# Optimization experiments

Hardware: AMD Instinct MI355X
Metric: run time of the kernel (lower is better)

## Reference

```python
import jax, jax.numpy as jnp
import numpy as np

HIDDEN = 1024
HEADS = 16
HEAD_DIM = HIDDEN // HEADS
B, L = 4, 2048


def setup_inputs() -> dict:
    key = jax.random.key(0)
    ks = jax.random.split(key, 9)
    s = 1.0 / np.sqrt(HIDDEN)
    inp = {
        "x": jax.random.normal(ks[0], (B, L, HIDDEN), dtype=jnp.float32),
        "wq": jax.random.uniform(ks[1], (HIDDEN, HIDDEN), jnp.float32, -s, s),
        "bq": jax.random.uniform(ks[2], (HIDDEN,), jnp.float32, -s, s),
        "wk": jax.random.uniform(ks[3], (HIDDEN, HIDDEN), jnp.float32, -s, s),
        "bk": jax.random.uniform(ks[4], (HIDDEN,), jnp.float32, -s, s),
        "wv": jax.random.uniform(ks[5], (HIDDEN, HIDDEN), jnp.float32, -s, s),
        "bv": jax.random.uniform(ks[6], (HIDDEN,), jnp.float32, -s, s),
        "wo": jax.random.uniform(ks[7], (HIDDEN, HIDDEN), jnp.float32, -s, s),
        "bo": jax.random.uniform(ks[8], (HIDDEN,), jnp.float32, -s, s),
    }
    return inp


def reference(x, wq, bq, wk, bk, wv, bv, wo, bo):
    b, l, d = x.shape
    # projections (torch Linear: x @ W^T + b; here weights stored as [in,out])
    q = x @ wq + bq
    k = x @ wk + bk
    v = x @ wv + bv
    # [b, h, l, hd]
    q = q.reshape(b, l, HEADS, HEAD_DIM).transpose(0, 2, 1, 3)
    k = k.reshape(b, l, HEADS, HEAD_DIM).transpose(0, 2, 1, 3)
    v = v.reshape(b, l, HEADS, HEAD_DIM).transpose(0, 2, 1, 3)
    scale = 1.0 / np.sqrt(HEAD_DIM).astype(np.float32)
    score = jnp.einsum('bhqd,bhkd->bhqk', q, k) * scale
    attn = jax.nn.softmax(score, axis=-1)
    out = jnp.einsum('bhqk,bhkd->bhqd', attn, v)
    out = out.transpose(0, 2, 1, 3).reshape(b, l, d)
    return out @ wo + bo
```

## Files before the change

kernel.cpp:

```cpp
#include <hip/hip_runtime.h>
#include <hip/hip_bf16.h>
#include <cstdint>

#define HIDDEN 1024
#define HEADS 16
#define HEAD_DIM 64
#define BATCH 4
#define SEQ 2048
#define TOK (BATCH * SEQ)

typedef __attribute__((ext_vector_type(8))) short short8;
typedef __attribute__((ext_vector_type(4))) float f32x4;
typedef __attribute__((ext_vector_type(16))) float f32x16;

__device__ __forceinline__ void gload_lds16(const void* g, void* s) {
  __builtin_amdgcn_global_load_lds(
      (const __attribute__((address_space(1))) void*)g,
      (__attribute__((address_space(3))) void*)s, 16, 0, 0);
}

__device__ __forceinline__ unsigned short f2bf(float x) {
  union { __hip_bfloat16 h; unsigned short u; } c;
  c.h = __float2bfloat16(x);
  return c.u;
}

__global__ __launch_bounds__(256) void convert_f32_bf16(
    const float* __restrict__ in, __hip_bfloat16* __restrict__ out, int n4) {
  int idx = blockIdx.x * blockDim.x + threadIdx.x;
  int stride = gridDim.x * blockDim.x;
  for (int i = idx; i < n4; i += stride) {
    float4 v = ((const float4*)in)[i];
    union { ushort4 u; __hip_bfloat16 h[4]; } r;
    r.h[0] = __float2bfloat16(v.x);
    r.h[1] = __float2bfloat16(v.y);
    r.h[2] = __float2bfloat16(v.z);
    r.h[3] = __float2bfloat16(v.w);
    ((ushort4*)out)[i] = r.u;
  }
}

__global__ __launch_bounds__(256) void transpose_to_bf16(
    const float* __restrict__ in, __hip_bfloat16* __restrict__ out) {
  __shared__ __hip_bfloat16 t[64][65];
  const int tx = threadIdx.x & 63;
  const int ty = threadIdx.x >> 6;
  const int k0 = blockIdx.y * 64;
  const int n0 = blockIdx.x * 64;
#pragma unroll
  for (int i = 0; i < 16; ++i) {
    int r = i * 4 + ty;
    t[r][tx] = __float2bfloat16(in[(size_t)(k0 + r) * 1024 + n0 + tx]);
  }
  __syncthreads();
#pragma unroll
  for (int i = 0; i < 16; ++i) {
    int r = i * 4 + ty;
    out[(size_t)(n0 + r) * 1024 + k0 + tx] = t[tx][r];
  }
}

template <int EPI, int KDIM>
__global__ __launch_bounds__(256) void gemm128(
    const __hip_bfloat16* __restrict__ A, const __hip_bfloat16* __restrict__ Bt,
    float* __restrict__ Cout, const float* __restrict__ bias,
    const float* __restrict__ bq, const float* __restrict__ bk,
    const float* __restrict__ bv, __hip_bfloat16* __restrict__ Qb,
    __hip_bfloat16* __restrict__ Kb, __hip_bfloat16* __restrict__ VTb) {
  __shared__ __hip_bfloat16 As[128 * 32];
  __shared__ __hip_bfloat16 Bs[128 * 32];
  const int tid = threadIdx.x;
  const int w = tid >> 6, l = tid & 63;
  const int lc = l & 15, lg = l >> 4;
  const int wr = w >> 1, wc = w & 1;
  const int bm0 = blockIdx.x * 128;
  const int bn0 = blockIdx.y * 128;
  const int lrow = l >> 2;
  const int lk = (l & 3) * 8;

  f32x4 acc[4][4] = {};

#pragma unroll 1
  for (int kt = 0; kt < KDIM; kt += 32) {
    if (w < 2) {
#pragma unroll
      for (int i = 0; i < 4; ++i) {
        int rloc = w * 64 + i * 16;
        const __hip_bfloat16* src =
            A + (size_t)(bm0 + rloc + lrow) * KDIM + kt + lk;
        gload_lds16(src, &As[rloc * 32]);
      }
    } else {
#pragma unroll
      for (int i = 0; i < 4; ++i) {
        int rloc = (w - 2) * 64 + i * 16;
        const __hip_bfloat16* src =
            Bt + (size_t)(bn0 + rloc + lrow) * KDIM + kt + lk;
        gload_lds16(src, &Bs[rloc * 32]);
      }
    }
    __syncthreads();
    short8 af[4], bf[4];
#pragma unroll
    for (int mt = 0; mt < 4; ++mt)
      af[mt] = *(const short8*)&As[(wr * 64 + mt * 16 + lc) * 32 + 8 * lg];
#pragma unroll
    for (int nt = 0; nt < 4; ++nt)
      bf[nt] = *(const short8*)&Bs[(wc * 64 + nt * 16 + lc) * 32 + 8 * lg];
#pragma unroll
    for (int mt = 0; mt < 4; ++mt)
#pragma unroll
      for (int nt = 0; nt < 4; ++nt)
        acc[mt][nt] = __builtin_amdgcn_mfma_f32_16x16x32_bf16(
            af[mt], bf[nt], acc[mt][nt], 0, 0, 0);
    __syncthreads();
  }

#pragma unroll
  for (int mt = 0; mt < 4; ++mt) {
#pragma unroll
    for (int nt = 0; nt < 4; ++nt) {
#pragma unroll
      for (int r = 0; r < 4; ++r) {
        int m = bm0 + wr * 64 + mt * 16 + 4 * lg + r;
        int n = bn0 + wc * 64 + nt * 16 + lc;
        float v = acc[mt][nt][r];
        if (EPI == 0) {
          Cout[(size_t)m * 1024 + n] = v + bias[n];
        } else {
          int proj = n >> 10, win = n & 1023, h = win >> 6, d = win & 63;
          const float* bp = (proj == 0) ? bq : ((proj == 1) ? bk : bv);
          __hip_bfloat16 hv = __float2bfloat16(v + bp[win]);
          int b = m >> 11, lq = m & 2047;
          if (proj == 0)
            Qb[((size_t)(b * 16 + h) * 2048 + lq) * 64 + d] = hv;
          else if (proj == 1)
            Kb[((size_t)(b * 16 + h) * 2048 + lq) * 64 + d] = hv;
          else
            VTb[((size_t)(b * 16 + h) * 64 + d) * 2048 + lq] = hv;
        }
      }
    }
  }
}

__global__ __launch_bounds__(256, 2) void attn32(
    const __hip_bfloat16* __restrict__ Qb, const __hip_bfloat16* __restrict__ Kb,
    const __hip_bfloat16* __restrict__ VTb, __hip_bfloat16* __restrict__ AO) {
  __shared__ __align__(16) char lds[2][2][8192];
  const int tid = threadIdx.x;
  const int w = tid >> 6, l = tid & 63;
  const int q32 = l & 31;
  const int hi = l >> 5;
  const int bh = blockIdx.y;
  const int qb = blockIdx.x;
  const int b = bh >> 4, h = bh & 15;

  const __hip_bfloat16* Qp = Qb + (size_t)bh * SEQ * 64;
  const char* Kg = (const char*)(Kb + (size_t)bh * SEQ * 64);
  const char* Vg = (const char*)(VTb + (size_t)bh * 64 * SEQ);

  const int q0w = qb * 128 + w * 32;
  short8 qf[4];
#pragma unroll
  for (int ds = 0; ds < 4; ++ds)
    qf[ds] = *(const short8*)(Qp + (size_t)(q0w + q32) * 64 + ds * 16 + 8 * hi);

  const int srow = l >> 3;
  const int scol = (16 * (l & 7)) ^ (srow << 4);
  const int i0 = 2 * w, i1 = 2 * w + 1;

#define STAGE_KV(buf, kv0)                                                   \
  {                                                                          \
    gload_lds16(Kg + (size_t)((kv0) + i0 * 8 + srow) * 128 + scol,           \
                &lds[buf][0][i0 * 1024]);                                    \
    gload_lds16(Kg + (size_t)((kv0) + i1 * 8 + srow) * 128 + scol,           \
                &lds[buf][0][i1 * 1024]);                                    \
    gload_lds16(Vg + (size_t)(i0 * 8 + srow) * (SEQ * 2) +                   \
                    (size_t)(kv0) * 2 + scol,                                \
                &lds[buf][1][i0 * 1024]);                                    \
    gload_lds16(Vg + (size_t)(i1 * 8 + srow) * (SEQ * 2) +                   \
                    (size_t)(kv0) * 2 + scol,                                \
                &lds[buf][1][i1 * 1024]);                                    \
  }

  STAGE_KV(0, 0);

  f32x16 o0 = {}, o1 = {};
  float mrun = -INFINITY, lrun = 0.0f;
  const float cs = 0.125f * 1.44269504088896f;
  const int swz = (q32 & 7) << 4;

#pragma unroll 1
  for (int it = 0; it < 32; ++it) {
    const int kv0 = it * 64;
    const int cur = it & 1;
    __syncthreads();
    if (it < 31) STAGE_KV(cur ^ 1, kv0 + 64);

    const char* Kt = lds[cur][0];
    f32x16 s0 = {}, s1 = {};
#pragma unroll
    for (int ds = 0; ds < 4; ++ds) {
      const int c = (32 * ds + 16 * hi) ^ swz;
      short8 k0 = *(const short8*)(Kt + q32 * 128 + c);
      short8 k1 = *(const short8*)(Kt + (32 + q32) * 128 + c);
      s0 = __builtin_amdgcn_mfma_f32_32x32x16_bf16(k0, qf[ds], s0, 0, 0, 0);
      s1 = __builtin_amdgcn_mfma_f32_32x32x16_bf16(k1, qf[ds], s1, 0, 0, 0);
    }

    float tm[8];
#pragma unroll
    for (int i = 0; i < 8; ++i)
      tm[i] = fmaxf(fmaxf(s0[2 * i], s0[2 * i + 1]),
                    fmaxf(s1[2 * i], s1[2 * i + 1]));
    float t = fmaxf(fmaxf(fmaxf(tm[0], tm[1]), fmaxf(tm[2], tm[3])),
                    fmaxf(fmaxf(tm[4], tm[5]), fmaxf(tm[6], tm[7])));
    t = fmaxf(t, __shfl_xor(t, 32));

    const float mn = fmaxf(mrun, t * cs);
    const float corr = exp2f(mrun - mn);
    mrun = mn;

    float p0[16], p1[16];
    float rs = 0.0f;
#pragma unroll
    for (int i = 0; i < 16; ++i) {
      p0[i] = exp2f(fmaf(s0[i], cs, -mn));
      p1[i] = exp2f(fmaf(s1[i], cs, -mn));
      rs += p0[i] + p1[i];
    }
    rs += __shfl_xor(rs, 32);
    lrun = lrun * corr + rs;

    uint32_t pw[4][4];
#pragma unroll
    for (int ks = 0; ks < 4; ++ks) {
      const int base = 8 * (ks & 1);
#pragma unroll
      for (int g = 0; g < 4; ++g) {
        float lo = (ks < 2) ? p0[base + 2 * g] : p1[base + 2 * g];
        float hp = (ks < 2) ? p0[base + 2 * g + 1] : p1[base + 2 * g + 1];
        pw[ks][g] = (uint32_t)f2bf(lo) | ((uint32_t)f2bf(hp) << 16);
      }
    }

    o0 *= corr;
    o1 *= corr;

    const char* Vt = lds[cur][1];
#pragma unroll
    for (int ks = 0; ks < 4; ++ks) {
      union { short8 v; uint32_t u[4]; } pb;
      pb.u[0] = pw[ks][0];
      pb.u[1] = pw[ks][1];
      pb.u[2] = pw[ks][2];
      pb.u[3] = pw[ks][3];
      const int cA = (32 * ks + 8 * hi) ^ swz;
      const int cB = (32 * ks + 16 + 8 * hi) ^ swz;
      union { short8 v; uint64_t u[2]; } a0, a1;
      a0.u[0] = *(const uint64_t*)(Vt + q32 * 128 + cA);
      a0.u[1] = *(const uint64_t*)(Vt + q32 * 128 + cB);
      a1.u[0] = *(const uint64_t*)(Vt + (32 + q32) * 128 + cA);
      a1.u[1] = *(const uint64_t*)(Vt + (32 + q32) * 128 + cB);
      o0 = __builtin_amdgcn_mfma_f32_32x32x16_bf16(a0.v, pb.v, o0, 0, 0, 0);
      o1 = __builtin_amdgcn_mfma_f32_32x32x16_bf16(a1.v, pb.v, o1, 0, 0, 0);
    }
  }

  const float rinv = 1.0f / lrun;
  const size_t orow = (size_t)(b * SEQ + q0w + q32) * 1024 + h * 64;
#pragma unroll
  for (int g = 0; g < 4; ++g) {
    ushort4 c0, c1;
    c0.x = f2bf(o0[4 * g + 0] * rinv);
    c0.y = f2bf(o0[4 * g + 1] * rinv);
    c0.z = f2bf(o0[4 * g + 2] * rinv);
    c0.w = f2bf(o0[4 * g + 3] * rinv);
    c1.x = f2bf(o1[4 * g + 0] * rinv);
    c1.y = f2bf(o1[4 * g + 1] * rinv);
    c1.z = f2bf(o1[4 * g + 2] * rinv);
    c1.w = f2bf(o1[4 * g + 3] * rinv);
    *(ushort4*)(AO + orow + 8 * g + 4 * hi) = c0;
    *(ushort4*)(AO + orow + 32 + 8 * g + 4 * hi) = c1;
  }
#undef STAGE_KV
}

extern "C" void kernel_launch(void* const* d_in, const int* in_sizes, int n_in,
                              void* d_out, int out_size, void* d_ws,
                              size_t ws_size, hipStream_t stream) {
  const float* x = (const float*)d_in[0];
  const float* wq = (const float*)d_in[1];
  const float* bq = (const float*)d_in[2];
  const float* wk = (const float*)d_in[3];
  const float* bk = (const float*)d_in[4];
  const float* wv = (const float*)d_in[5];
  const float* bv = (const float*)d_in[6];
  const float* wo = (const float*)d_in[7];
  const float* bo = (const float*)d_in[8];
  float* out = (float*)d_out;
  char* ws = (char*)d_ws;

  __hip_bfloat16* XB = (__hip_bfloat16*)(ws);
  __hip_bfloat16* WT = (__hip_bfloat16*)(ws + (16ull << 20));
  __hip_bfloat16* WOT = (__hip_bfloat16*)(ws + (22ull << 20));
  __hip_bfloat16* QB = (__hip_bfloat16*)(ws + (24ull << 20));
  __hip_bfloat16* KB = (__hip_bfloat16*)(ws + (40ull << 20));
  __hip_bfloat16* VTB = (__hip_bfloat16*)(ws + (56ull << 20));
  __hip_bfloat16* AO = XB;

  convert_f32_bf16<<<2048, 256, 0, stream>>>(x, XB, TOK * HIDDEN / 4);
  transpose_to_bf16<<<dim3(16, 16), 256, 0, stream>>>(wq, WT);
  transpose_to_bf16<<<dim3(16, 16), 256, 0, stream>>>(wk, WT + 1024 * 1024);
  transpose_to_bf16<<<dim3(16, 16), 256, 0, stream>>>(wv, WT + 2 * 1024 * 1024);
  transpose_to_bf16<<<dim3(16, 16), 256, 0, stream>>>(wo, WOT);

  gemm128<1, 1024><<<dim3(64, 24), 256, 0, stream>>>(
      XB, WT, nullptr, nullptr, bq, bk, bv, QB, KB, VTB);

  attn32<<<dim3(16, 64), 256, 0, stream>>>(QB, KB, VTB, AO);

  gemm128<0, 1024><<<dim3(64, 8), 256, 0, stream>>>(
      AO, WOT, out, bo, nullptr, nullptr, nullptr, nullptr, nullptr, nullptr);
}
```

Before: 368.6 us.

## Lazy softmax rescale, packed bf16 converts, max3 reductions, higher attention occupancy

The attention kernel skips the running-max update and the output/denominator rescale when every lane's new tile max stays within 8 (log2 units) of the running max, using a wave vote. Probability and output bf16 packing switches to the hardware v_cvt_pk_bf16_f32 instruction, and the max reduction is restructured into three-input max chains. Launch bounds are raised from 2 to 4 blocks per CU. Together these aim to cut VALU work in the softmax path, at the cost of possible register pressure or spills from the tighter occupancy bound and larger exponent values (up to 2^8) before normalisation.

Result: faster. 349.4 us (-5.2%).

```diff
diff --git a/kernel.cpp b/kernel.cpp
--- a/kernel.cpp
+++ b/kernel.cpp
@@ -23,6 +23,12 @@
   union { __hip_bfloat16 h; unsigned short u; } c;
   c.h = __float2bfloat16(x);
   return c.u;
+}
+
+__device__ __forceinline__ uint32_t cvt_pk_bf16(float lo, float hi) {
+  uint32_t r;
+  asm("v_cvt_pk_bf16_f32 %0, %1, %2" : "=v"(r) : "v"(lo), "v"(hi));
+  return r;
 }
 
 __global__ __launch_bounds__(256) void convert_f32_bf16(
@@ -144,7 +150,7 @@
   }
 }
 
-__global__ __launch_bounds__(256, 2) void attn32(
+__global__ __launch_bounds__(256, 4) void attn32(
     const __hip_bfloat16* __restrict__ Qb, const __hip_bfloat16* __restrict__ Kb,
     const __hip_bfloat16* __restrict__ VTb, __hip_bfloat16* __restrict__ AO) {
   __shared__ __align__(16) char lds[2][2][8192];
@@ -209,18 +215,26 @@
       s1 = __builtin_amdgcn_mfma_f32_32x32x16_bf16(k1, qf[ds], s1, 0, 0, 0);
     }
 
-    float tm[8];
-#pragma unroll
-    for (int i = 0; i < 8; ++i)
-      tm[i] = fmaxf(fmaxf(s0[2 * i], s0[2 * i + 1]),
-                    fmaxf(s1[2 * i], s1[2 * i + 1]));
-    float t = fmaxf(fmaxf(fmaxf(tm[0], tm[1]), fmaxf(tm[2], tm[3])),
-                    fmaxf(fmaxf(tm[4], tm[5]), fmaxf(tm[6], tm[7])));
+#define M3F(a, b, c) fmaxf(fmaxf((a), (b)), (c))
+    float u0 = M3F(s0[0], s0[1], s0[2]);
+    float u1 = M3F(s0[3], s0[4], s0[5]);
+    float u2 = M3F(s0[6], s0[7], s0[8]);
+    float u3 = M3F(s0[9], s0[10], s0[11]);
+    float u4 = M3F(s0[12], s0[13], s0[14]);
+    float u5 = M3F(s0[15], s1[0], s1[1]);
+    float u6 = M3F(s1[2], s1[3], s1[4]);
+    float u7 = M3F(s1[5], s1[6], s1[7]);
+    float u8 = M3F(s1[8], s1[9], s1[10]);
+    float u9 = M3F(s1[11], s1[12], s1[13]);
+    float ua = fmaxf(s1[14], s1[15]);
+    float t =
+        M3F(M3F(u0, u1, u2), M3F(u3, u4, u5), M3F(M3F(u6, u7, u8), u9, ua));
+#undef M3F
     t = fmaxf(t, __shfl_xor(t, 32));
-
-    const float mn = fmaxf(mrun, t * cs);
-    const float corr = exp2f(mrun - mn);
-    mrun = mn;
+    const float tl = t * cs;
+
+    const bool nores = (__all(tl <= mrun + 8.0f) != 0);
+    const float mn = nores ? mrun : fmaxf(mrun, tl);
 
     float p0[16], p1[16];
     float rs = 0.0f;
@@ -231,7 +245,15 @@
       rs += p0[i] + p1[i];
     }
     rs += __shfl_xor(rs, 32);
-    lrun = lrun * corr + rs;
+
+    if (!nores) {
+      const float corr = exp2f(mrun - mn);
+      mrun = mn;
+      lrun *= corr;
+      o0 *= corr;
+      o1 *= corr;
+    }
+    lrun += rs;
 
     uint32_t pw[4][4];
 #pragma unroll
@@ -241,12 +263,9 @@
       for (int g = 0; g < 4; ++g) {
         float lo = (ks < 2) ? p0[base + 2 * g] : p1[base + 2 * g];
         float hp = (ks < 2) ? p0[base + 2 * g + 1] : p1[base + 2 * g + 1];
-        pw[ks][g] = (uint32_t)f2bf(lo) | ((uint32_t)f2bf(hp) << 16);
+        pw[ks][g] = cvt_pk_bf16(lo, hp);
       }
     }
-
-    o0 *= corr;
-    o1 *= corr;
 
     const char* Vt = lds[cur][1];
 #pragma unroll
@@ -272,17 +291,13 @@
   const size_t orow = (size_t)(b * SEQ + q0w + q32) * 1024 + h * 64;
 #pragma unroll
   for (int g = 0; g < 4; ++g) {
-    ushort4 c0, c1;
-    c0.x = f2bf(o0[4 * g + 0] * rinv);
-    c0.y = f2bf(o0[4 * g + 1] * rinv);
-    c0.z = f2bf(o0[4 * g + 2] * rinv);
-    c0.w = f2bf(o0[4 * g + 3] * rinv);
-    c1.x = f2bf(o1[4 * g + 0] * rinv);
-    c1.y = f2bf(o1[4 * g + 1] * rinv);
-    c1.z = f2bf(o1[4 * g + 2] * rinv);
-    c1.w = f2bf(o1[4 * g + 3] * rinv);
-    *(ushort4*)(AO + orow + 8 * g + 4 * hi) = c0;
-    *(ushort4*)(AO + orow + 32 + 8 * g + 4 * hi) = c1;
+    uint2 wa, wb;
+    wa.x = cvt_pk_bf16(o0[4 * g + 0] * rinv, o0[4 * g + 1] * rinv);
+    wa.y = cvt_pk_bf16(o0[4 * g + 2] * rinv, o0[4 * g + 3] * rinv);
+    wb.x = cvt_pk_bf16(o1[4 * g + 0] * rinv, o1[4 * g + 1] * rinv);
+    wb.y = cvt_pk_bf16(o1[4 * g + 2] * rinv, o1[4 * g + 3] * rinv);
+    *(uint2*)(AO + orow + 8 * g + 4 * hi) = wa;
+    *(uint2*)(AO + orow + 32 + 8 * g + 4 * hi) = wb;
   }
 #undef STAGE_KV
 }
```
